# Kernel optimization log

Measured on AMD Instinct MI355X. Metric: run time of the kernel, lower is better.

Reference implementation:

```python
import jax, jax.numpy as jnp
import numpy as np

N = 100000
E = 1600000
D_IN = 64
D_OUT = 64


def setup_inputs() -> dict:
    key = jax.random.key(0)
    k1, k2, k3, k4, k5 = jax.random.split(key, 5)
    x = jax.random.normal(k1, (N, D_IN), dtype=jnp.float32)
    edge_index = jax.random.randint(k2, (2, E), 0, N, dtype=jnp.int64)
    edge_attr = jax.random.uniform(k3, (E,), dtype=jnp.float32)
    # GraphConv params: lin_rel (with bias) applied to aggregated messages,
    # lin_root (no bias) applied to root/self features.
    scale = 1.0 / np.sqrt(D_IN)
    W_rel = jax.random.uniform(k4, (D_OUT, D_IN), dtype=jnp.float32, minval=-scale, maxval=scale)
    b_rel = jnp.zeros((D_OUT,), dtype=jnp.float32)
    W_root = jax.random.uniform(k5, (D_OUT, D_IN), dtype=jnp.float32, minval=-scale, maxval=scale)
    return {"x": x, "edge_index": edge_index, "edge_attr": edge_attr,
            "W_rel": W_rel, "b_rel": b_rel, "W_root": W_root}


def reference(x, edge_index, edge_attr, W_rel, b_rel, W_root):
    src = edge_index[0]  # message sources (x_j)
    dst = edge_index[1]  # message targets (aggregation index)
    # message: x_j * edge_weight, then sum-aggregate at target nodes
    msgs = x[src] * edge_attr[:, None]                     # [E, D_IN]
    agg = jax.ops.segment_sum(msgs, dst, num_segments=N)   # [N, D_IN]
    # GraphConv: lin_rel(agg) + lin_root(x)
    out = agg @ W_rel.T + b_rel + x @ W_root.T             # [N, D_OUT]
    return jax.nn.relu(out)
```

## Files before the change

### kernel.cpp

```cpp
#include <hip/hip_runtime.h>
#include <hip/hip_bf16.h>

#define N_NODES 100000
#define N_EDGES 1600000
#define D 64
#define SLOT 48
#define WSCALE 32767.0f

#define BSHIFT 8
#define BNODES 256
#define NB 391
#define CAP_B 4672
#define CHUNK 4096
#define NBIN_BLOCKS ((N_EDGES + CHUNK - 1) / CHUNK)

#define BPT 512
#define PREP_BLOCKS (N_NODES * D / 4 / BPT)
#define FUSED_GRID (NBIN_BLOCKS + PREP_BLOCKS + 1)

__device__ inline ushort f2bu(float f) {
    __hip_bfloat16 h = __float2bfloat16(f);
    return *(ushort*)&h;
}

__global__ __launch_bounds__(BPT) void bin_prep_kernel(
    const int* __restrict__ src,
    const int* __restrict__ dst,
    const float* __restrict__ w,
    int* __restrict__ gcur,
    int2* __restrict__ bucketed,
    const float* __restrict__ x,
    ushort* __restrict__ xb,
    const float* __restrict__ Wrel,
    const float* __restrict__ Wroot,
    ushort* __restrict__ wb)
{
    __shared__ int h[NB];
    __shared__ int cur[NB];
    __shared__ int sdst[CHUNK];
    int tid = threadIdx.x;

    if (blockIdx.x >= NBIN_BLOCKS) {
        int pb = blockIdx.x - NBIN_BLOCKS;
        if (pb == PREP_BLOCKS) {
            for (int i = tid; i < 2 * D * D; i += BPT) {
                float f = (i < D * D) ? Wrel[i] : Wroot[i - D * D];
                wb[i] = f2bu(f);
            }
        } else {
            int i = (pb * BPT + tid) * 4;
            float4 v = *(const float4*)(x + i);
            ushort4 o;
            o.x = f2bu(v.x); o.y = f2bu(v.y); o.z = f2bu(v.z); o.w = f2bu(v.w);
            *(ushort4*)(xb + i) = o;
        }
        return;
    }

    for (int b = tid; b < NB; b += BPT) h[b] = 0;
    __syncthreads();

    int e0 = blockIdx.x * CHUNK;
    for (int i = tid; i < CHUNK; i += BPT) {
        int e = e0 + i;
        int d = (e < N_EDGES) ? dst[e] : -1;
        sdst[i] = d;
        if (d >= 0) atomicAdd(&h[d >> BSHIFT], 1);
    }
    __syncthreads();

    for (int b = tid; b < NB; b += BPT) {
        int c = h[b];
        cur[b] = (c > 0) ? atomicAdd(&gcur[b], c) : 0;
    }
    __syncthreads();

    for (int i = tid; i < CHUNK; i += BPT) {
        int e = e0 + i;
        int d = sdst[i];
        if (d >= 0) {
            int b = d >> BSHIFT;
            int p = atomicAdd(&cur[b], 1);
            int q = (int)(w[e] * WSCALE + 0.5f);
            q = min(q, 32767);
            unsigned pk = (unsigned)src[e] | ((unsigned)q << 17);
            if (p < CAP_B)
                bucketed[(size_t)b * CAP_B + p] = make_int2((int)pk, d & (BNODES - 1));
        }
    }
}

#define FG_T 512

__global__ __launch_bounds__(FG_T) void fill_gather_kernel(
    const int* __restrict__ gcur,
    const int2* __restrict__ bucketed,
    const ushort* __restrict__ xb,
    ushort* __restrict__ aggb)
{
    __shared__ int lcnt[BNODES];
    __shared__ unsigned __align__(16) img[BNODES * SLOT];
    int tid = threadIdx.x;
    int b   = blockIdx.x;

    for (int i = tid; i < BNODES; i += FG_T) lcnt[i] = 0;
    __syncthreads();

    int nE = min(gcur[b], CAP_B);
    const int2* __restrict__ be = bucketed + (size_t)b * CAP_B;
    for (int i = tid; i < nE; i += FG_T) {
        int2 v = be[i];
        int p = atomicAdd(&lcnt[v.y], 1);
        if (p < SLOT)
            img[v.y * SLOT + p] = (unsigned)v.x;
    }
    __syncthreads();

    int g = tid >> 3;
    int t = tid & 7;

    for (int n = g; n < BNODES; n += 64) {
        int node = b * BNODES + n;
        if (node >= N_NODES) break;
        int dg = min(lcnt[n], SLOT);
        const unsigned* __restrict__ row = &img[n * SLOT];

        float a0 = 0.f, a1 = 0.f, a2 = 0.f, a3 = 0.f;
        float a4 = 0.f, a5 = 0.f, a6 = 0.f, a7 = 0.f;
#pragma unroll 2
        for (int j = 0; j < dg; ++j) {
            unsigned v = row[j];
            int s = v & 0x1FFFF;
            float wv = (float)(v >> 17) * (1.0f / WSCALE);
            uint4 dx = *(const uint4*)(xb + (size_t)s * D + 8 * t);
            a0 += __uint_as_float(dx.x << 16)         * wv;
            a1 += __uint_as_float(dx.x & 0xFFFF0000u) * wv;
            a2 += __uint_as_float(dx.y << 16)         * wv;
            a3 += __uint_as_float(dx.y & 0xFFFF0000u) * wv;
            a4 += __uint_as_float(dx.z << 16)         * wv;
            a5 += __uint_as_float(dx.z & 0xFFFF0000u) * wv;
            a6 += __uint_as_float(dx.w << 16)         * wv;
            a7 += __uint_as_float(dx.w & 0xFFFF0000u) * wv;
        }

        union { ushort u[8]; uint4 q; } pk;
        pk.u[0] = f2bu(a0); pk.u[1] = f2bu(a1);
        pk.u[2] = f2bu(a2); pk.u[3] = f2bu(a3);
        pk.u[4] = f2bu(a4); pk.u[5] = f2bu(a5);
        pk.u[6] = f2bu(a6); pk.u[7] = f2bu(a7);
        *(uint4*)(aggb + (size_t)node * D + 8 * t) = pk.q;
    }
}

typedef __attribute__((ext_vector_type(8))) short bf8;
typedef __attribute__((ext_vector_type(4))) float f4;

__global__ __launch_bounds__(256) void linear_kernel(
    const ushort* __restrict__ xb,
    const ushort* __restrict__ aggb,
    float* __restrict__ out,
    const ushort* __restrict__ wb,
    const float* __restrict__ brel)
{
    __shared__ float __align__(16) sOut[4][16][68];

    int tid  = threadIdx.x;
    int wv   = tid >> 6, lane = tid & 63;
    int node0 = (blockIdx.x * 4 + wv) * 16;
    if (node0 >= N_NODES) return;

    int m    = lane & 15;
    int quad = lane >> 4;

    bf8 bw[2][4][2];
#pragma unroll
    for (int mat = 0; mat < 2; ++mat)
#pragma unroll
        for (int nt = 0; nt < 4; ++nt)
#pragma unroll
            for (int s = 0; s < 2; ++s)
                bw[mat][nt][s] = *(const bf8*)(wb + mat * D * D
                                               + (16 * nt + m) * 64 + s * 32 + quad * 8);

    const ushort* ar = aggb + (size_t)(node0 + m) * 64 + quad * 8;
    bf8 aagg0 = *(const bf8*)ar;
    bf8 aagg1 = *(const bf8*)(ar + 32);
    const ushort* xr = xb + (size_t)(node0 + m) * 64 + quad * 8;
    bf8 ax0 = *(const bf8*)xr;
    bf8 ax1 = *(const bf8*)(xr + 32);

    f4 acc[4];
#pragma unroll
    for (int nt = 0; nt < 4; ++nt) {
        float b = brel[16 * nt + m];
        f4 c = {b, b, b, b};
        c = __builtin_amdgcn_mfma_f32_16x16x32_bf16(aagg0, bw[0][nt][0], c, 0, 0, 0);
        c = __builtin_amdgcn_mfma_f32_16x16x32_bf16(aagg1, bw[0][nt][1], c, 0, 0, 0);
        c = __builtin_amdgcn_mfma_f32_16x16x32_bf16(ax0,   bw[1][nt][0], c, 0, 0, 0);
        c = __builtin_amdgcn_mfma_f32_16x16x32_bf16(ax1,   bw[1][nt][1], c, 0, 0, 0);
        acc[nt] = c;
    }

#pragma unroll
    for (int nt = 0; nt < 4; ++nt)
#pragma unroll
        for (int r = 0; r < 4; ++r)
            sOut[wv][quad * 4 + r][16 * nt + m] = fmaxf(acc[nt][r], 0.f);
#pragma unroll
    for (int p = 0; p < 4; ++p) {
        int idx = p * 64 + lane;
        int row = idx >> 4;
        int c4  = (idx & 15) * 4;
        float4 v = *(const float4*)&sOut[wv][row][c4];
        *(float4*)(out + (size_t)(node0 + row) * 64 + c4) = v;
    }
}

extern "C" void kernel_launch(void* const* d_in, const int* in_sizes, int n_in,
                              void* d_out, int out_size, void* d_ws, size_t ws_size,
                              hipStream_t stream)
{
    const float* x     = (const float*)d_in[0];
    const int*   eidx  = (const int*)d_in[1];
    const float* eattr = (const float*)d_in[2];
    const float* Wrel  = (const float*)d_in[3];
    const float* brel  = (const float*)d_in[4];
    const float* Wroot = (const float*)d_in[5];
    float* out = (float*)d_out;

    const int* src = eidx;
    const int* dst = eidx + N_EDGES;

    int*      gcur     = (int*)d_ws;
    int2*     bucketed = (int2*)(gcur + 1024);
    ushort*   xb       = (ushort*)(bucketed + (size_t)NB * CAP_B);
    ushort*   wb       = xb + (size_t)N_NODES * D;
    ushort*   aggb     = wb + 2 * D * D;

    hipMemsetAsync(gcur, 0, NB * sizeof(int), stream);

    bin_prep_kernel<<<FUSED_GRID, BPT, 0, stream>>>(src, dst, eattr, gcur, bucketed,
                                                    x, xb, Wrel, Wroot, wb);
    fill_gather_kernel<<<NB, FG_T, 0, stream>>>(gcur, bucketed, xb, aggb);
    linear_kernel<<<(N_NODES + 63) / 64, 256, 0, stream>>>(xb, aggb, out, wb, brel);
}
```

Before: 165.4 us.

## Fuse the bf16 MFMA linear layer into the gather kernel epilogue

The separate linear kernel is merged into the gather kernel. After each block has aggregated its 256 nodes, its 8 waves each run the MFMA GEMM on two 16-node tiles, reading the freshly written aggregated rows back through cache. The output staging buffer shares shared memory with the edge image through a union, and weights are loaded per tile instead of held in registers. This removes one kernel launch and the cold global re-read of the aggregated features, but the GEMM now runs on only 391 blocks, and the added launch-bounds occupancy hint may limit registers.

```diff
diff --git a/kernel.cpp b/kernel.cpp
--- a/kernel.cpp
+++ b/kernel.cpp
@@ -92,14 +92,23 @@
 
 #define FG_T 512
 
-__global__ __launch_bounds__(FG_T) void fill_gather_kernel(
+typedef __attribute__((ext_vector_type(8))) short bf8;
+typedef __attribute__((ext_vector_type(4))) float f4;
+
+__global__ __launch_bounds__(FG_T, 6) void gather_linear_kernel(
     const int* __restrict__ gcur,
     const int2* __restrict__ bucketed,
     const ushort* __restrict__ xb,
-    ushort* __restrict__ aggb)
+    ushort* __restrict__ aggb,
+    const ushort* __restrict__ wb,
+    const float* __restrict__ brel,
+    float* __restrict__ out)
 {
     __shared__ int lcnt[BNODES];
-    __shared__ unsigned __align__(16) img[BNODES * SLOT];
+    __shared__ union __align__(16) {
+        unsigned img[BNODES * SLOT];
+        float sOut[8][16][68];
+    } u;
     int tid = threadIdx.x;
     int b   = blockIdx.x;
 
@@ -112,7 +121,7 @@
         int2 v = be[i];
         int p = atomicAdd(&lcnt[v.y], 1);
         if (p < SLOT)
-            img[v.y * SLOT + p] = (unsigned)v.x;
+            u.img[v.y * SLOT + p] = (unsigned)v.x;
     }
     __syncthreads();
 
@@ -123,7 +132,7 @@
         int node = b * BNODES + n;
         if (node >= N_NODES) break;
         int dg = min(lcnt[n], SLOT);
-        const unsigned* __restrict__ row = &img[n * SLOT];
+        const unsigned* __restrict__ row = &u.img[n * SLOT];
 
         float a0 = 0.f, a1 = 0.f, a2 = 0.f, a3 = 0.f;
         float a4 = 0.f, a5 = 0.f, a6 = 0.f, a7 = 0.f;
@@ -143,76 +152,62 @@
             a7 += __uint_as_float(dx.w & 0xFFFF0000u) * wv;
         }
 
-        union { ushort u[8]; uint4 q; } pk;
-        pk.u[0] = f2bu(a0); pk.u[1] = f2bu(a1);
-        pk.u[2] = f2bu(a2); pk.u[3] = f2bu(a3);
-        pk.u[4] = f2bu(a4); pk.u[5] = f2bu(a5);
-        pk.u[6] = f2bu(a6); pk.u[7] = f2bu(a7);
+        union { ushort u16[8]; uint4 q; } pk;
+        pk.u16[0] = f2bu(a0); pk.u16[1] = f2bu(a1);
+        pk.u16[2] = f2bu(a2); pk.u16[3] = f2bu(a3);
+        pk.u16[4] = f2bu(a4); pk.u16[5] = f2bu(a5);
+        pk.u16[6] = f2bu(a6); pk.u16[7] = f2bu(a7);
         *(uint4*)(aggb + (size_t)node * D + 8 * t) = pk.q;
     }
-}
-
-typedef __attribute__((ext_vector_type(8))) short bf8;
-typedef __attribute__((ext_vector_type(4))) float f4;
-
-__global__ __launch_bounds__(256) void linear_kernel(
-    const ushort* __restrict__ xb,
-    const ushort* __restrict__ aggb,
-    float* __restrict__ out,
-    const ushort* __restrict__ wb,
-    const float* __restrict__ brel)
-{
-    __shared__ float __align__(16) sOut[4][16][68];
-
-    int tid  = threadIdx.x;
+    __syncthreads();
+
     int wv   = tid >> 6, lane = tid & 63;
-    int node0 = (blockIdx.x * 4 + wv) * 16;
-    if (node0 >= N_NODES) return;
-
     int m    = lane & 15;
     int quad = lane >> 4;
 
-    bf8 bw[2][4][2];
-#pragma unroll
-    for (int mat = 0; mat < 2; ++mat)
+#pragma unroll
+    for (int tt = 0; tt < 2; ++tt) {
+        int tile  = wv * 2 + tt;
+        int node0 = b * BNODES + tile * 16;
+        if (node0 >= N_NODES) break;
+
+        const ushort* ar = aggb + (size_t)(node0 + m) * D + quad * 8;
+        bf8 aagg0 = *(const bf8*)ar;
+        bf8 aagg1 = *(const bf8*)(ar + 32);
+        const ushort* xr = xb + (size_t)(node0 + m) * D + quad * 8;
+        bf8 ax0 = *(const bf8*)xr;
+        bf8 ax1 = *(const bf8*)(xr + 32);
+
+        f4 acc[4];
+#pragma unroll
+        for (int nt = 0; nt < 4; ++nt) {
+            const ushort* wr = wb + (16 * nt + m) * D + quad * 8;
+            bf8 b00 = *(const bf8*)(wr);
+            bf8 b01 = *(const bf8*)(wr + 32);
+            bf8 b10 = *(const bf8*)(wr + D * D);
+            bf8 b11 = *(const bf8*)(wr + D * D + 32);
+            float bb = brel[16 * nt + m];
+            f4 c = {bb, bb, bb, bb};
+            c = __builtin_amdgcn_mfma_f32_16x16x32_bf16(aagg0, b00, c, 0, 0, 0);
+            c = __builtin_amdgcn_mfma_f32_16x16x32_bf16(aagg1, b01, c, 0, 0, 0);
+            c = __builtin_amdgcn_mfma_f32_16x16x32_bf16(ax0,   b10, c, 0, 0, 0);
+            c = __builtin_amdgcn_mfma_f32_16x16x32_bf16(ax1,   b11, c, 0, 0, 0);
+            acc[nt] = c;
+        }
+
 #pragma unroll
         for (int nt = 0; nt < 4; ++nt)
 #pragma unroll
-            for (int s = 0; s < 2; ++s)
-                bw[mat][nt][s] = *(const bf8*)(wb + mat * D * D
-                                               + (16 * nt + m) * 64 + s * 32 + quad * 8);
-
-    const ushort* ar = aggb + (size_t)(node0 + m) * 64 + quad * 8;
-    bf8 aagg0 = *(const bf8*)ar;
-    bf8 aagg1 = *(const bf8*)(ar + 32);
-    const ushort* xr = xb + (size_t)(node0 + m) * 64 + quad * 8;
-    bf8 ax0 = *(const bf8*)xr;
-    bf8 ax1 = *(const bf8*)(xr + 32);
-
-    f4 acc[4];
-#pragma unroll
-    for (int nt = 0; nt < 4; ++nt) {
-        float b = brel[16 * nt + m];
-        f4 c = {b, b, b, b};
-        c = __builtin_amdgcn_mfma_f32_16x16x32_bf16(aagg0, bw[0][nt][0], c, 0, 0, 0);
-        c = __builtin_amdgcn_mfma_f32_16x16x32_bf16(aagg1, bw[0][nt][1], c, 0, 0, 0);
-        c = __builtin_amdgcn_mfma_f32_16x16x32_bf16(ax0,   bw[1][nt][0], c, 0, 0, 0);
-        c = __builtin_amdgcn_mfma_f32_16x16x32_bf16(ax1,   bw[1][nt][1], c, 0, 0, 0);
-        acc[nt] = c;
-    }
-
-#pragma unroll
-    for (int nt = 0; nt < 4; ++nt)
-#pragma unroll
-        for (int r = 0; r < 4; ++r)
-            sOut[wv][quad * 4 + r][16 * nt + m] = fmaxf(acc[nt][r], 0.f);
-#pragma unroll
-    for (int p = 0; p < 4; ++p) {
-        int idx = p * 64 + lane;
-        int row = idx >> 4;
-        int c4  = (idx & 15) * 4;
-        float4 v = *(const float4*)&sOut[wv][row][c4];
-        *(float4*)(out + (size_t)(node0 + row) * 64 + c4) = v;
+            for (int r = 0; r < 4; ++r)
+                u.sOut[wv][quad * 4 + r][16 * nt + m] = fmaxf(acc[nt][r], 0.f);
+#pragma unroll
+        for (int p = 0; p < 4; ++p) {
+            int idx = p * 64 + lane;
+            int row = idx >> 4;
+            int c4  = (idx & 15) * 4;
+            float4 v = *(const float4*)&u.sOut[wv][row][c4];
+            *(float4*)(out + (size_t)(node0 + row) * D + c4) = v;
+        }
     }
 }
 
@@ -241,6 +236,5 @@
 
     bin_prep_kernel<<<FUSED_GRID, BPT, 0, stream>>>(src, dst, eattr, gcur, bucketed,
                                                     x, xb, Wrel, Wroot, wb);
-    fill_gather_kernel<<<NB, FG_T, 0, stream>>>(gcur, bucketed, xb, aggb);
-    linear_kernel<<<(N_NODES + 63) / 64, 256, 0, stream>>>(xb, aggb, out, wb, brel);
-}
+    gather_linear_kernel<<<NB, FG_T, 0, stream>>>(gcur, bucketed, xb, aggb, wb, brel, out);
+}
```

Measured after the change: 170.8 us. 1.03x slower.

## Stage binned edges in shared memory to coalesce bucket scatter writes

Applied to the files above, without the earlier changes.

The binning kernel now does a block-local prefix scan over bucket counts, scatters the packed edges into a shared-memory staging buffer sorted by bucket, and then writes them to global memory in bucket-contiguous runs. Edge loads for dst, src and weight are also hoisted into registers with clamped indices, so each edge is read once. The aim is to replace scattered 8-byte global stores with mostly contiguous ones. In exchange it adds a log-step scan with many barriers and uses 32KB more shared memory per block, which may lower occupancy.

```diff
diff --git a/kernel.cpp b/kernel.cpp
--- a/kernel.cpp
+++ b/kernel.cpp
@@ -15,6 +15,7 @@
 #define NBIN_BLOCKS ((N_EDGES + CHUNK - 1) / CHUNK)
 
 #define BPT 512
+#define EPT (CHUNK / BPT)
 #define PREP_BLOCKS (N_NODES * D / 4 / BPT)
 #define FUSED_GRID (NBIN_BLOCKS + PREP_BLOCKS + 1)
 
@@ -36,8 +37,10 @@
     ushort* __restrict__ wb)
 {
     __shared__ int h[NB];
+    __shared__ int sc[BPT];
     __shared__ int cur[NB];
-    __shared__ int sdst[CHUNK];
+    __shared__ int gbase[NB];
+    __shared__ int2 sbuf[CHUNK];
     int tid = threadIdx.x;
 
     if (blockIdx.x >= NBIN_BLOCKS) {
@@ -61,32 +64,57 @@
     __syncthreads();
 
     int e0 = blockIdx.x * CHUNK;
-    for (int i = tid; i < CHUNK; i += BPT) {
-        int e = e0 + i;
-        int d = (e < N_EDGES) ? dst[e] : -1;
-        sdst[i] = d;
-        if (d >= 0) atomicAdd(&h[d >> BSHIFT], 1);
-    }
-    __syncthreads();
-
-    for (int b = tid; b < NB; b += BPT) {
-        int c = h[b];
-        cur[b] = (c > 0) ? atomicAdd(&gcur[b], c) : 0;
-    }
-    __syncthreads();
-
-    for (int i = tid; i < CHUNK; i += BPT) {
-        int e = e0 + i;
-        int d = sdst[i];
-        if (d >= 0) {
-            int b = d >> BSHIFT;
+    int d[EPT], pk[EPT];
+#pragma unroll
+    for (int k = 0; k < EPT; ++k) {
+        int e  = e0 + k * BPT + tid;
+        int ec = min(e, N_EDGES - 1);
+        int dd = dst[ec];
+        int q  = (int)(w[ec] * WSCALE + 0.5f);
+        q = min(q, 32767);
+        pk[k] = src[ec] | (q << 17);
+        d[k]  = (e < N_EDGES) ? dd : -1;
+        if (d[k] >= 0) atomicAdd(&h[dd >> BSHIFT], 1);
+    }
+    __syncthreads();
+
+    sc[tid] = (tid < NB) ? h[tid] : 0;
+    __syncthreads();
+#pragma unroll
+    for (int off = 1; off < BPT; off <<= 1) {
+        int v = sc[tid];
+        int u = (tid >= off) ? sc[tid - off] : 0;
+        __syncthreads();
+        sc[tid] = v + u;
+        __syncthreads();
+    }
+
+    if (tid < NB) {
+        int c = h[tid];
+        gbase[tid] = (c > 0) ? atomicAdd(&gcur[tid], c) : 0;
+        cur[tid]   = (tid > 0) ? sc[tid - 1] : 0;
+    }
+    __syncthreads();
+
+#pragma unroll
+    for (int k = 0; k < EPT; ++k) {
+        if (d[k] >= 0) {
+            int b = d[k] >> BSHIFT;
             int p = atomicAdd(&cur[b], 1);
-            int q = (int)(w[e] * WSCALE + 0.5f);
-            q = min(q, 32767);
-            unsigned pk = (unsigned)src[e] | ((unsigned)q << 17);
-            if (p < CAP_B)
-                bucketed[(size_t)b * CAP_B + p] = make_int2((int)pk, d & (BNODES - 1));
+            sbuf[p] = make_int2(pk[k], d[k]);
         }
+    }
+    __syncthreads();
+
+    int total = sc[NB - 1];
+    for (int i = tid; i < total; i += BPT) {
+        int2 v   = sbuf[i];
+        int dd   = v.y;
+        int b    = dd >> BSHIFT;
+        int excl = (b > 0) ? sc[b - 1] : 0;
+        int gpos = gbase[b] + (i - excl);
+        if (gpos < CAP_B)
+            bucketed[(size_t)b * CAP_B + gpos] = make_int2(v.x, dd & (BNODES - 1));
     }
 }
 
```

After: 161.0 us. 2.6% less time.
